# Kernel optimization log

Hardware: AMD Instinct MI355X
Metric: run time of the kernel (lower is better)

The kernel has to match this reference:

```python
import jax, jax.numpy as jnp
import numpy as np

ALPHA = 0.5  # default alpha of convex_ssd_chunk_forward
B_SZ, H, CS, DH, DS = 16, 32, 256, 64, 128


def setup_inputs() -> dict:
    key = jax.random.key(0)
    k1, k2, k3, k4, k5 = jax.random.split(key, 5)
    # A_chunk holds per-step log-decays; must be <= 0 so exp(cumsum) stays bounded.
    A_chunk = -jax.random.uniform(k2, (B_SZ, H, CS), dtype=jnp.float32) * 0.1
    return {
        "X_chunk": jax.random.normal(k1, (B_SZ, H, CS, DH), dtype=jnp.float32),
        "A_chunk": A_chunk,
        "B_chunk": jax.random.normal(k3, (B_SZ, H, CS, DS), dtype=jnp.float32),
        "C_chunk": jax.random.normal(k4, (B_SZ, H, CS, DS), dtype=jnp.float32),
        "h_prev": jax.random.normal(k5, (B_SZ, H, DS, DH), dtype=jnp.float32),
    }


def reference(X_chunk, A_chunk, B_chunk, C_chunk, h_prev):
    # Mamba2 SSD chunk scan with convex-combination state update.
    # X_chunk: [b,h,cs,dh], A_chunk: [b,h,cs], B/C_chunk: [b,h,cs,ds], h_prev: [b,h,ds,dh]
    cs = X_chunk.shape[2]
    A_cumsum = jnp.cumsum(A_chunk, axis=-1)                      # [b,h,cs]
    # Causal decay matrix L[i,j] = exp(Acum[i]-Acum[j]) for i>=j, else 0.
    diff = A_cumsum[..., :, None] - A_cumsum[..., None, :]       # [b,h,cs,cs]
    causal = jnp.tril(jnp.ones((cs, cs), dtype=bool))
    L = jnp.where(causal, jnp.exp(diff), 0.0)
    CB = jnp.einsum('bhid,bhjd->bhij', C_chunk, B_chunk)         # [b,h,cs,cs]
    Y_intra = jnp.einsum('bhij,bhjd->bhid', L * CB, X_chunk)     # [b,h,cs,dh]
    decay_to_end = jnp.exp(A_cumsum[:, :, -1:] - A_cumsum)       # [b,h,cs]
    h_chunk_contrib = jnp.einsum('bhts,bhtd,bht->bhsd', B_chunk, X_chunk, decay_to_end)  # [b,h,ds,dh]
    decay_total = jnp.exp(A_cumsum[:, :, -1])                    # [b,h]
    h_prev_decayed = decay_total[..., None, None] * h_prev
    h_end = ALPHA * h_prev_decayed + (1.0 - ALPHA) * h_chunk_contrib
    decay_from_start = jnp.exp(A_cumsum)                         # [b,h,cs]
    Y_inter = ALPHA * jnp.einsum('bhis,bhsd,bhi->bhid', C_chunk, h_prev, decay_from_start)
    Y_chunk = (1.0 - ALPHA) * Y_intra + Y_inter                  # [b,h,cs,dh]
    return Y_chunk, h_end, decay_total
```

## Files before the change

### kernel.cpp

```cpp
#include <hip/hip_runtime.h>

typedef __attribute__((ext_vector_type(8))) short s16x8;
typedef __attribute__((ext_vector_type(4))) float f32x4;
typedef __attribute__((ext_vector_type(4))) unsigned u32x4;

namespace {
constexpr int kCS = 256, kDH = 64, kDS = 128, kBH = 512;
constexpr float kAlpha = 0.5f;

constexpr int OFF_AC   = 0;
constexpr int OFF_ENEG = 1024;
constexpr int OFF_B    = 2048;
constexpr int OFF_BLO  = OFF_B + 8192;
constexpr int OFF_XT   = OFF_B + 16384;
constexpr int OFF_XTLO = OFF_XT + 4096;
constexpr int OFF_S    = OFF_XTLO + 4096;
constexpr int LDS_BYTES = OFF_S + 8192;

constexpr int HOFF_BT   = 2048;
constexpr int HOFF_BTLO = HOFF_BT + 8192;
constexpr int HOFF_XT   = HOFF_BT + 16384;
constexpr int HOFF_XTLO = HOFF_XT + 4096;
}

union F4 { float4 v; float f[4]; };

__device__ __forceinline__ unsigned cvt_pk_bf16(float a, float b) {
  unsigned r;
  asm("v_cvt_pk_bf16_f32 %0, %1, %2" : "=v"(r) : "v"(a), "v"(b));
  return r;
}

__device__ __forceinline__ unsigned short bf16_1(float x) {
  return (unsigned short)cvt_pk_bf16(x, x);
}

__device__ __forceinline__ void split2(float a, float b, unsigned& h, unsigned& l) {
  h = cvt_pk_bf16(a, b);
  l = cvt_pk_bf16(a - __uint_as_float(h << 16), b - __uint_as_float(h & 0xFFFF0000u));
}

__device__ __forceinline__ void split8v(float4 a, float4 b, s16x8& hi, s16x8& lo) {
  unsigned h0, h1, h2, h3, l0, l1, l2, l3;
  split2(a.x, a.y, h0, l0);
  split2(a.z, a.w, h1, l1);
  split2(b.x, b.y, h2, l2);
  split2(b.z, b.w, h3, l3);
  u32x4 H = {h0, h1, h2, h3}, L = {l0, l1, l2, l3};
  hi = __builtin_bit_cast(s16x8, H);
  lo = __builtin_bit_cast(s16x8, L);
}

__device__ __forceinline__ void split8s(float x0, float x1, float x2, float x3,
                                        float x4, float x5, float x6, float x7,
                                        s16x8& hi, s16x8& lo) {
  unsigned h0, h1, h2, h3, l0, l1, l2, l3;
  split2(x0, x1, h0, l0);
  split2(x2, x3, h1, l1);
  split2(x4, x5, h2, l2);
  split2(x6, x7, h3, l3);
  u32x4 H = {h0, h1, h2, h3}, L = {l0, l1, l2, l3};
  hi = __builtin_bit_cast(s16x8, H);
  lo = __builtin_bit_cast(s16x8, L);
}

__device__ __forceinline__ void lds_barrier() {
  asm volatile("s_waitcnt lgkmcnt(0)" ::: "memory");
  __builtin_amdgcn_s_barrier();
  __builtin_amdgcn_sched_barrier(0);
}

__global__ __launch_bounds__(512, 4) void fused_kernel(
    const float* __restrict__ Xg, const float* __restrict__ Ag,
    const float* __restrict__ Bg, const float* __restrict__ Cg,
    const float* __restrict__ Hg, float* __restrict__ Yg,
    float* __restrict__ hend, float* __restrict__ dtot) {
  __shared__ __align__(16) char smem[LDS_BYTES];
  const int bidx = blockIdx.x;
  const int tid = threadIdx.x;
  const int lane = tid & 63;
  const int w = tid >> 6;
  const int fr = lane & 15;
  const int fg = lane >> 4;

  const int swz = (bidx & 7) * 192 + (bidx >> 3);
  const int role = swz % 3;
  const int bh = swz / 3;

  const float* Xb = Xg + (size_t)bh * kCS * kDH;
  const float* Ab = Ag + (size_t)bh * kCS;
  const float* Bb = Bg + (size_t)bh * kCS * kDS;
  const float* Hb = Hg + (size_t)bh * kDS * kDH;

  if (role == 2) {
    float* ac   = (float*)(smem + OFF_AC);
    short* BThi = (short*)(smem + HOFF_BT);
    short* BTlo = (short*)(smem + HOFF_BTLO);
    short* XThi = (short*)(smem + HOFF_XT);
    short* XTlo = (short*)(smem + HOFF_XTLO);
    float* Ob = hend + (size_t)bh * kDS * kDH;

    float v = 0.f;
    if (tid < 256) {
      v = Ab[tid];
#pragma unroll
      for (int off = 1; off < 64; off <<= 1) {
        float t = __shfl_up(v, off);
        if (lane >= off) v += t;
      }
      float* wsum = (float*)(smem + HOFF_BT);
      if (lane == 63) wsum[w] = v;
    }
    __syncthreads();
    if (tid < 256) {
      const float* wsum = (const float*)(smem + HOFF_BT);
      float base = 0.f;
#pragma unroll
      for (int k = 0; k < 4; ++k)
        if (k < w) base += wsum[k];
      ac[tid] = v + base;
    }
    __syncthreads();
    const float alast = ac[kCS - 1];
    if (tid == 0) dtot[bh] = __expf(alast);

    f32x4 acc[4];
#pragma unroll
    for (int dg = 0; dg < 4; ++dg)
#pragma unroll
      for (int r = 0; r < 4; ++r) acc[dg][r] = 0.f;

    const int sblk = tid & 31;
    const int tq = (tid >> 5) & 7;
    const int st = w * 16 + fr;

    for (int t0 = 0; t0 < kCS; t0 += 32) {
      if (tid < 256) {
        F4 hr[4];
#pragma unroll
        for (int r = 0; r < 4; ++r)
          hr[r].v = *(const float4*)&Bb[(size_t)(t0 + tq * 4 + r) * kDS + sblk * 4];
#pragma unroll
        for (int c = 0; c < 4; ++c) {
          const int s2 = sblk * 4 + c;
          unsigned h0, h1, l0, l1;
          split2(hr[0].f[c], hr[1].f[c], h0, l0);
          split2(hr[2].f[c], hr[3].f[c], h1, l1);
          const int off = s2 * 32 + (((tq >> 1) ^ ((s2 >> 2) & 3)) << 3) + ((tq & 1) << 2);
          ((unsigned*)&BThi[off])[0] = h0;
          ((unsigned*)&BThi[off])[1] = h1;
          ((unsigned*)&BTlo[off])[0] = l0;
          ((unsigned*)&BTlo[off])[1] = l1;
        }
      } else {
        const int t2 = tid - 256;
        const int d = t2 & 63;
        const int wx = t2 >> 6;
        const float* xp = &Xb[(size_t)(t0 + wx * 8) * kDH + d];
        const float* ap = &ac[t0 + wx * 8];
        float w0 = __expf(alast - ap[0]), w1 = __expf(alast - ap[1]);
        float w2 = __expf(alast - ap[2]), w3 = __expf(alast - ap[3]);
        float w4 = __expf(alast - ap[4]), w5 = __expf(alast - ap[5]);
        float w6 = __expf(alast - ap[6]), w7 = __expf(alast - ap[7]);
        s16x8 h8, l8;
        split8s(xp[0 * kDH] * w0, xp[1 * kDH] * w1, xp[2 * kDH] * w2, xp[3 * kDH] * w3,
                xp[4 * kDH] * w4, xp[5 * kDH] * w5, xp[6 * kDH] * w6, xp[7 * kDH] * w7,
                h8, l8);
        const int off = d * 32 + ((wx ^ ((d >> 2) & 3)) << 3);
        *(s16x8*)&XThi[off] = h8;
        *(s16x8*)&XTlo[off] = l8;
      }
      __syncthreads();
      const int aoff = st * 32 + ((fg ^ ((st >> 2) & 3)) << 3);
      s16x8 ah = *(const s16x8*)&BThi[aoff];
      s16x8 al = *(const s16x8*)&BTlo[aoff];
#pragma unroll
      for (int dg = 0; dg < 4; ++dg) {
        const int drow = dg * 16 + fr;
        const int xoff = drow * 32 + ((fg ^ ((drow >> 2) & 3)) << 3);
        s16x8 xh = *(const s16x8*)&XThi[xoff];
        s16x8 xl = *(const s16x8*)&XTlo[xoff];
        acc[dg] = __builtin_amdgcn_mfma_f32_16x16x32_bf16(ah, xh, acc[dg], 0, 0, 0);
        acc[dg] = __builtin_amdgcn_mfma_f32_16x16x32_bf16(ah, xl, acc[dg], 0, 0, 0);
        acc[dg] = __builtin_amdgcn_mfma_f32_16x16x32_bf16(al, xh, acc[dg], 0, 0, 0);
      }
      __syncthreads();
    }
    const float dscale = kAlpha * __expf(alast);
    const float sc = 1.f - kAlpha;
#pragma unroll
    for (int dg = 0; dg < 4; ++dg) {
#pragma unroll
      for (int r = 0; r < 4; ++r) {
        const int s = w * 16 + fg * 4 + r;
        const int d = dg * 16 + fr;
        Ob[(size_t)s * kDH + d] = dscale * Hb[(size_t)s * kDH + d] + sc * acc[dg][r];
      }
    }
    return;
  }

  const int itA = role;
  const int itB = 3 - role;
  const int i0A = itA * 64, i0B = itB * 64;
  const int jt_n = 2 * itB + 2;
  const int jtA_n = 2 * itA + 2;
  const bool gB = w >= 4;
  const int wl = w & 3;
  const int i0g = gB ? i0B : i0A;

  float* ac   = (float*)(smem + OFF_AC);
  float* eneg = (float*)(smem + OFF_ENEG);
  short* Bhi  = (short*)(smem + OFF_B);
  short* Blo  = (short*)(smem + OFF_BLO);
  short* XThi = (short*)(smem + OFF_XT);
  short* XTlo = (short*)(smem + OFF_XTLO);
  short* Sall = (short*)(smem + OFF_S);
  float* CbA  = (float*)(smem + OFF_B);
  float* CbB  = (float*)(smem + OFF_XT);
  short* HThi = (short*)(smem + OFF_B);
  short* HTlo = (short*)(smem + OFF_XT);

  const float* Cg_b = Cg + (size_t)bh * kCS * kDS;
  float* Yb = Yg + (size_t)bh * kCS * kDH;

  {
    float v = 0.f;
    if (tid < 256) {
      v = Ab[tid];
#pragma unroll
      for (int off = 1; off < 64; off <<= 1) {
        float t = __shfl_up(v, off);
        if (lane >= off) v += t;
      }
      float* wsum = (float*)(smem + OFF_S);
      if (lane == 63) wsum[w] = v;
    }
    __syncthreads();
    if (tid < 256) {
      const float* wsum = (const float*)(smem + OFF_S);
      float base = 0.f;
#pragma unroll
      for (int k = 0; k < 4; ++k)
        if (k < w) base += wsum[k];
      const float a = v + base;
      ac[tid] = a;
      eneg[tid] = __expf(-a);
    }
    __syncthreads();
  }

  float eaci[4];
#pragma unroll
  for (int r = 0; r < 4; ++r) eaci[r] = __expf(ac[i0g + wl * 16 + fg * 4 + r]);

  const int prow = (tid >> 4) & 15;
  const int pg = tid & 15;
  const int xd = (tid - 256) & 63;
  const int xw = ((tid - 256) >> 6) & 3;
  float4 pb0, pb1, pb2, pb3;
  float px0, px1, px2, px3, px4, px5, px6, px7;
  if (tid < 256) {
    pb0 = *(const float4*)&Bb[(size_t)prow * kDS + pg * 8];
    pb1 = *(const float4*)&Bb[(size_t)prow * kDS + pg * 8 + 4];
    pb2 = *(const float4*)&Bb[(size_t)(16 + prow) * kDS + pg * 8];
    pb3 = *(const float4*)&Bb[(size_t)(16 + prow) * kDS + pg * 8 + 4];
  } else {
    const float* xp = &Xb[(size_t)(xw * 8) * kDH + xd];
    px0 = xp[0 * kDH]; px1 = xp[1 * kDH]; px2 = xp[2 * kDH]; px3 = xp[3 * kDH];
    px4 = xp[4 * kDH]; px5 = xp[5 * kDH]; px6 = xp[6 * kDH]; px7 = xp[7 * kDH];
  }

  s16x8 chi[4], clo[4];
#pragma unroll
  for (int m = 0; m < 2; ++m) {
#pragma unroll
    for (int k = 0; k < 2; ++k) {
      int fid = k * 512 + tid;
      int r = fid >> 5, c = fid & 31;
      *(float4*)&CbA[r * 128 + ((c ^ (r & 7)) << 2)] =
          *(const float4*)&Cg_b[(size_t)(i0A + m * 32 + r) * kDS + c * 4];
      *(float4*)&CbB[r * 128 + ((c ^ (r & 7)) << 2)] =
          *(const float4*)&Cg_b[(size_t)(i0B + m * 32 + r) * kDS + c * 4];
    }
    __syncthreads();
    if ((wl >> 1) == m) {
      const int lrow = (wl & 1) * 16 + fr;
      const float* crow = (gB ? CbB : CbA) + lrow * 128;
      const int r7 = lrow & 7;
#pragma unroll
      for (int kc = 0; kc < 4; ++kc) {
        const int c0 = kc * 8 + fg * 2;
        F4 u0, u1;
        u0.v = *(const float4*)&crow[(c0 ^ r7) << 2];
        u1.v = *(const float4*)&crow[((c0 + 1) ^ r7) << 2];
        split8v(u0.v, u1.v, chi[kc], clo[kc]);
      }
    }
    __syncthreads();
  }

  f32x4 yacc[4];
#pragma unroll
  for (int n = 0; n < 4; ++n)
#pragma unroll
    for (int r = 0; r < 4; ++r) yacc[n][r] = 0.f;

  short* Sp = Sall + w * 512;

  for (int jt = 0; jt < jt_n; ++jt) {
    if (tid < 256) {
      s16x8 h8, l8;
      split8v(pb0, pb1, h8, l8);
      int col = (pg ^ (prow & 7)) * 8;
      *(s16x8*)&Bhi[prow * 128 + col] = h8;
      *(s16x8*)&Blo[prow * 128 + col] = l8;
      const int row1 = 16 + prow;
      split8v(pb2, pb3, h8, l8);
      col = (pg ^ (row1 & 7)) * 8;
      *(s16x8*)&Bhi[row1 * 128 + col] = h8;
      *(s16x8*)&Blo[row1 * 128 + col] = l8;
    } else {
      s16x8 h8, l8;
      split8s(px0, px1, px2, px3, px4, px5, px6, px7, h8, l8);
      const int off = xd * 32 + ((xw ^ ((xd >> 2) & 3)) << 3);
      *(s16x8*)&XThi[off] = h8;
      *(s16x8*)&XTlo[off] = l8;
    }
    if (jt + 1 < jt_n) {
      const int j0n = (jt + 1) * 32;
      if (tid < 256) {
        pb0 = *(const float4*)&Bb[(size_t)(j0n + prow) * kDS + pg * 8];
        pb1 = *(const float4*)&Bb[(size_t)(j0n + prow) * kDS + pg * 8 + 4];
        pb2 = *(const float4*)&Bb[(size_t)(j0n + 16 + prow) * kDS + pg * 8];
        pb3 = *(const float4*)&Bb[(size_t)(j0n + 16 + prow) * kDS + pg * 8 + 4];
      } else {
        const float* xp = &Xb[(size_t)(j0n + xw * 8) * kDH + xd];
        px0 = xp[0 * kDH]; px1 = xp[1 * kDH]; px2 = xp[2 * kDH]; px3 = xp[3 * kDH];
        px4 = xp[4 * kDH]; px5 = xp[5 * kDH]; px6 = xp[6 * kDH]; px7 = xp[7 * kDH];
      }
    }
    lds_barrier();

    if (gB || jt < jtA_n) {
      const int j0 = jt * 32;
      f32x4 sA[2], sB[2];
#pragma unroll
      for (int n = 0; n < 2; ++n) {
#pragma unroll
        for (int r = 0; r < 4; ++r) { sA[n][r] = 0.f; sB[n][r] = 0.f; }
        const int jrow = n * 16 + fr;
        const short* bph = &Bhi[jrow * 128];
        const short* bpl = &Blo[jrow * 128];
#pragma unroll
        for (int kc = 0; kc < 2; ++kc) {
          const int phys = ((4 * kc + fg) ^ (jrow & 7)) * 8;
          s16x8 b8 = *(const s16x8*)&bph[phys];
          s16x8 l8 = *(const s16x8*)&bpl[phys];
          sA[n] = __builtin_amdgcn_mfma_f32_16x16x32_bf16(chi[kc], b8, sA[n], 0, 0, 0);
          sA[n] = __builtin_amdgcn_mfma_f32_16x16x32_bf16(chi[kc], l8, sA[n], 0, 0, 0);
          sA[n] = __builtin_amdgcn_mfma_f32_16x16x32_bf16(clo[kc], b8, sA[n], 0, 0, 0);
        }
#pragma unroll
        for (int kc = 2; kc < 4; ++kc) {
          const int phys = ((4 * kc + fg) ^ (jrow & 7)) * 8;
          s16x8 b8 = *(const s16x8*)&bph[phys];
          s16x8 l8 = *(const s16x8*)&bpl[phys];
          sB[n] = __builtin_amdgcn_mfma_f32_16x16x32_bf16(chi[kc], b8, sB[n], 0, 0, 0);
          sB[n] = __builtin_amdgcn_mfma_f32_16x16x32_bf16(chi[kc], l8, sB[n], 0, 0, 0);
          sB[n] = __builtin_amdgcn_mfma_f32_16x16x32_bf16(clo[kc], b8, sB[n], 0, 0, 0);
        }
      }
#pragma unroll
      for (int n = 0; n < 2; ++n) {
        const int jg = j0 + n * 16 + fr;
        const float enj = eneg[jg];
#pragma unroll
        for (int r = 0; r < 4; ++r) {
          const int iwl = fg * 4 + r;
          const int ig = i0g + wl * 16 + iwl;
          float sv = (sA[n][r] + sB[n][r]) * eaci[r] * enj;
          sv = (jg <= ig) ? sv : 0.f;
          Sp[iwl * 32 + (((n * 2 + (fr >> 3)) ^ fg) << 3) + (fr & 7)] = (short)bf16_1(sv);
        }
      }
      {
        s16x8 sa = *(const s16x8*)&Sp[fr * 32 + ((fg ^ (fr >> 2)) << 3)];
#pragma unroll
        for (int n = 0; n < 4; ++n) {
          const int drow = n * 16 + fr;
          const int pxo = (fg ^ ((drow >> 2) & 3)) << 3;
          s16x8 xh = *(const s16x8*)&XThi[drow * 32 + pxo];
          s16x8 xl = *(const s16x8*)&XTlo[drow * 32 + pxo];
          yacc[n] = __builtin_amdgcn_mfma_f32_16x16x32_bf16(sa, xh, yacc[n], 0, 0, 0);
          yacc[n] = __builtin_amdgcn_mfma_f32_16x16x32_bf16(sa, xl, yacc[n], 0, 0, 0);
        }
      }
    }
    lds_barrier();
  }

  {
    const int dd = tid & 15, tt = tid >> 4;
    F4 hr[4];
#pragma unroll
    for (int r = 0; r < 4; ++r)
      hr[r].v = *(const float4*)&Hb[(size_t)(tt * 4 + r) * kDH + dd * 4];
#pragma unroll
    for (int c = 0; c < 4; ++c) {
      const int d = dd * 4 + c;
      unsigned h0, h1, l0, l1;
      split2(hr[0].f[c], hr[1].f[c], h0, l0);
      split2(hr[2].f[c], hr[3].f[c], h1, l1);
      const int off = d * 128 + (((tt >> 1) ^ (d & 7)) << 3) + ((tt & 1) << 2);
      ((unsigned*)&HThi[off])[0] = h0;
      ((unsigned*)&HThi[off])[1] = h1;
      ((unsigned*)&HTlo[off])[0] = l0;
      ((unsigned*)&HTlo[off])[1] = l1;
    }
  }
  __syncthreads();

  f32x4 yh[4];
#pragma unroll
  for (int n = 0; n < 4; ++n)
#pragma unroll
    for (int r = 0; r < 4; ++r) yh[n][r] = 0.f;

#pragma unroll
  for (int kc = 0; kc < 4; ++kc) {
#pragma unroll
    for (int n = 0; n < 4; ++n) {
      const int drow = n * 16 + fr;
      const int phys = ((4 * kc + fg) ^ (drow & 7)) * 8;
      s16x8 hh = *(const s16x8*)&HThi[drow * 128 + phys];
      s16x8 hl = *(const s16x8*)&HTlo[drow * 128 + phys];
      yh[n] = __builtin_amdgcn_mfma_f32_16x16x32_bf16(chi[kc], hh, yh[n], 0, 0, 0);
      yh[n] = __builtin_amdgcn_mfma_f32_16x16x32_bf16(chi[kc], hl, yh[n], 0, 0, 0);
      yh[n] = __builtin_amdgcn_mfma_f32_16x16x32_bf16(clo[kc], hh, yh[n], 0, 0, 0);
    }
  }

#pragma unroll
  for (int n = 0; n < 4; ++n) {
#pragma unroll
    for (int r = 0; r < 4; ++r) {
      const int ig = i0g + wl * 16 + fg * 4 + r;
      const int d = n * 16 + fr;
      Yb[(size_t)ig * kDH + d] = (1.f - kAlpha) * yacc[n][r] + (kAlpha * eaci[r]) * yh[n][r];
    }
  }
}

extern "C" void kernel_launch(void* const* d_in, const int* in_sizes, int n_in,
                              void* d_out, int out_size, void* d_ws, size_t ws_size,
                              hipStream_t stream) {
  const float* X = (const float*)d_in[0];
  const float* A = (const float*)d_in[1];
  const float* B = (const float*)d_in[2];
  const float* C = (const float*)d_in[3];
  const float* H = (const float*)d_in[4];
  float* out = (float*)d_out;
  float* Y = out;
  float* hend = Y + (size_t)kBH * kCS * kDH;
  float* dt = hend + (size_t)kBH * kDS * kDH;

  fused_kernel<<<1536, 512, 0, stream>>>(X, A, B, C, H, Y, hend, dt);
}
```

Before: 79.57 us.

## Merge Y row-tile blocks into one block per head with 32-row warp tiles

Replaces the three-role split, where two Y blocks each took two 64-row tiles per head plus one h_end block, with a single Y block per head. Each warp now owns two 16-row groups, and warps are paired (rb = w or 11-w) to balance the causal triangle. C fragments load directly from global memory into registers instead of being staged through LDS, and B/X tiles are streamed across all 8 j-tiles by every thread. This cuts the grid from 1536 to 1024 blocks and avoids reloading B/X twice per head, at the cost of more registers per warp and a longer serial loop per block.

```diff
diff --git a/kernel.cpp b/kernel.cpp
--- a/kernel.cpp
+++ b/kernel.cpp
@@ -83,16 +83,15 @@
   const int fr = lane & 15;
   const int fg = lane >> 4;
 
-  const int swz = (bidx & 7) * 192 + (bidx >> 3);
-  const int role = swz % 3;
-  const int bh = swz / 3;
+  const int p = bidx & 511;
+  const int bh = (p & 7) * 64 + (p >> 3);
 
   const float* Xb = Xg + (size_t)bh * kCS * kDH;
   const float* Ab = Ag + (size_t)bh * kCS;
   const float* Bb = Bg + (size_t)bh * kCS * kDS;
   const float* Hb = Hg + (size_t)bh * kDS * kDH;
 
-  if (role == 2) {
+  if (bidx >= 512) {
     float* ac   = (float*)(smem + OFF_AC);
     short* BThi = (short*)(smem + HOFF_BT);
     short* BTlo = (short*)(smem + HOFF_BTLO);
@@ -200,14 +199,8 @@
     return;
   }
 
-  const int itA = role;
-  const int itB = 3 - role;
-  const int i0A = itA * 64, i0B = itB * 64;
-  const int jt_n = 2 * itB + 2;
-  const int jtA_n = 2 * itA + 2;
-  const bool gB = w >= 4;
-  const int wl = w & 3;
-  const int i0g = gB ? i0B : i0A;
+  const int rb = (w < 4) ? w : (11 - w);
+  const int i0g = rb * 32;
 
   float* ac   = (float*)(smem + OFF_AC);
   float* eneg = (float*)(smem + OFF_ENEG);
@@ -216,8 +209,6 @@
   short* XThi = (short*)(smem + OFF_XT);
   short* XTlo = (short*)(smem + OFF_XTLO);
   short* Sall = (short*)(smem + OFF_S);
-  float* CbA  = (float*)(smem + OFF_B);
-  float* CbB  = (float*)(smem + OFF_XT);
   short* HThi = (short*)(smem + OFF_B);
   short* HTlo = (short*)(smem + OFF_XT);
 
@@ -250,156 +241,138 @@
     __syncthreads();
   }
 
-  float eaci[4];
-#pragma unroll
-  for (int r = 0; r < 4; ++r) eaci[r] = __expf(ac[i0g + wl * 16 + fg * 4 + r]);
-
-  const int prow = (tid >> 4) & 15;
-  const int pg = tid & 15;
-  const int xd = (tid - 256) & 63;
-  const int xw = ((tid - 256) >> 6) & 3;
-  float4 pb0, pb1, pb2, pb3;
-  float px0, px1, px2, px3, px4, px5, px6, px7;
-  if (tid < 256) {
-    pb0 = *(const float4*)&Bb[(size_t)prow * kDS + pg * 8];
-    pb1 = *(const float4*)&Bb[(size_t)prow * kDS + pg * 8 + 4];
-    pb2 = *(const float4*)&Bb[(size_t)(16 + prow) * kDS + pg * 8];
-    pb3 = *(const float4*)&Bb[(size_t)(16 + prow) * kDS + pg * 8 + 4];
-  } else {
-    const float* xp = &Xb[(size_t)(xw * 8) * kDH + xd];
+  float eaci[2][4];
+#pragma unroll
+  for (int g = 0; g < 2; ++g)
+#pragma unroll
+    for (int r = 0; r < 4; ++r)
+      eaci[g][r] = __expf(ac[i0g + g * 16 + fg * 4 + r]);
+
+  s16x8 chi[2][4], clo[2][4];
+#pragma unroll
+  for (int g = 0; g < 2; ++g) {
+    const float* crow = &Cg_b[(size_t)(i0g + g * 16 + fr) * kDS];
+#pragma unroll
+    for (int kc = 0; kc < 4; ++kc) {
+      F4 u0, u1;
+      u0.v = *(const float4*)&crow[kc * 32 + fg * 8];
+      u1.v = *(const float4*)&crow[kc * 32 + fg * 8 + 4];
+      split8v(u0.v, u1.v, chi[g][kc], clo[g][kc]);
+    }
+  }
+
+  const int brow = tid >> 4;
+  const int bg = tid & 15;
+  const int xd = lane;
+  const int xq = w;
+  float4 pb0, pb1;
+  float px0, px1, px2, px3;
+  {
+    pb0 = *(const float4*)&Bb[(size_t)brow * kDS + bg * 8];
+    pb1 = *(const float4*)&Bb[(size_t)brow * kDS + bg * 8 + 4];
+    const float* xp = &Xb[(size_t)(xq * 4) * kDH + xd];
     px0 = xp[0 * kDH]; px1 = xp[1 * kDH]; px2 = xp[2 * kDH]; px3 = xp[3 * kDH];
-    px4 = xp[4 * kDH]; px5 = xp[5 * kDH]; px6 = xp[6 * kDH]; px7 = xp[7 * kDH];
-  }
-
-  s16x8 chi[4], clo[4];
-#pragma unroll
-  for (int m = 0; m < 2; ++m) {
-#pragma unroll
-    for (int k = 0; k < 2; ++k) {
-      int fid = k * 512 + tid;
-      int r = fid >> 5, c = fid & 31;
-      *(float4*)&CbA[r * 128 + ((c ^ (r & 7)) << 2)] =
-          *(const float4*)&Cg_b[(size_t)(i0A + m * 32 + r) * kDS + c * 4];
-      *(float4*)&CbB[r * 128 + ((c ^ (r & 7)) << 2)] =
-          *(const float4*)&Cg_b[(size_t)(i0B + m * 32 + r) * kDS + c * 4];
-    }
-    __syncthreads();
-    if ((wl >> 1) == m) {
-      const int lrow = (wl & 1) * 16 + fr;
-      const float* crow = (gB ? CbB : CbA) + lrow * 128;
-      const int r7 = lrow & 7;
-#pragma unroll
-      for (int kc = 0; kc < 4; ++kc) {
-        const int c0 = kc * 8 + fg * 2;
-        F4 u0, u1;
-        u0.v = *(const float4*)&crow[(c0 ^ r7) << 2];
-        u1.v = *(const float4*)&crow[((c0 + 1) ^ r7) << 2];
-        split8v(u0.v, u1.v, chi[kc], clo[kc]);
-      }
-    }
-    __syncthreads();
-  }
-
-  f32x4 yacc[4];
-#pragma unroll
-  for (int n = 0; n < 4; ++n)
-#pragma unroll
-    for (int r = 0; r < 4; ++r) yacc[n][r] = 0.f;
+  }
+
+  f32x4 yacc[2][4];
+#pragma unroll
+  for (int g = 0; g < 2; ++g)
+#pragma unroll
+    for (int n = 0; n < 4; ++n)
+#pragma unroll
+      for (int r = 0; r < 4; ++r) yacc[g][n][r] = 0.f;
 
   short* Sp = Sall + w * 512;
 
-  for (int jt = 0; jt < jt_n; ++jt) {
-    if (tid < 256) {
+  for (int jt = 0; jt < 8; ++jt) {
+    {
       s16x8 h8, l8;
       split8v(pb0, pb1, h8, l8);
-      int col = (pg ^ (prow & 7)) * 8;
-      *(s16x8*)&Bhi[prow * 128 + col] = h8;
-      *(s16x8*)&Blo[prow * 128 + col] = l8;
-      const int row1 = 16 + prow;
-      split8v(pb2, pb3, h8, l8);
-      col = (pg ^ (row1 & 7)) * 8;
-      *(s16x8*)&Bhi[row1 * 128 + col] = h8;
-      *(s16x8*)&Blo[row1 * 128 + col] = l8;
-    } else {
-      s16x8 h8, l8;
-      split8s(px0, px1, px2, px3, px4, px5, px6, px7, h8, l8);
-      const int off = xd * 32 + ((xw ^ ((xd >> 2) & 3)) << 3);
-      *(s16x8*)&XThi[off] = h8;
-      *(s16x8*)&XTlo[off] = l8;
-    }
-    if (jt + 1 < jt_n) {
+      const int col = (bg ^ (brow & 7)) * 8;
+      *(s16x8*)&Bhi[brow * 128 + col] = h8;
+      *(s16x8*)&Blo[brow * 128 + col] = l8;
+    }
+    {
+      unsigned h0, h1, l0, l1;
+      split2(px0, px1, h0, l0);
+      split2(px2, px3, h1, l1);
+      const int off = xd * 32 + (((xq >> 1) ^ ((xd >> 2) & 3)) << 3) + ((xq & 1) << 2);
+      ((unsigned*)&XThi[off])[0] = h0;
+      ((unsigned*)&XThi[off])[1] = h1;
+      ((unsigned*)&XTlo[off])[0] = l0;
+      ((unsigned*)&XTlo[off])[1] = l1;
+    }
+    if (jt + 1 < 8) {
       const int j0n = (jt + 1) * 32;
-      if (tid < 256) {
-        pb0 = *(const float4*)&Bb[(size_t)(j0n + prow) * kDS + pg * 8];
-        pb1 = *(const float4*)&Bb[(size_t)(j0n + prow) * kDS + pg * 8 + 4];
-        pb2 = *(const float4*)&Bb[(size_t)(j0n + 16 + prow) * kDS + pg * 8];
-        pb3 = *(const float4*)&Bb[(size_t)(j0n + 16 + prow) * kDS + pg * 8 + 4];
-      } else {
-        const float* xp = &Xb[(size_t)(j0n + xw * 8) * kDH + xd];
-        px0 = xp[0 * kDH]; px1 = xp[1 * kDH]; px2 = xp[2 * kDH]; px3 = xp[3 * kDH];
-        px4 = xp[4 * kDH]; px5 = xp[5 * kDH]; px6 = xp[6 * kDH]; px7 = xp[7 * kDH];
-      }
+      pb0 = *(const float4*)&Bb[(size_t)(j0n + brow) * kDS + bg * 8];
+      pb1 = *(const float4*)&Bb[(size_t)(j0n + brow) * kDS + bg * 8 + 4];
+      const float* xp = &Xb[(size_t)(j0n + xq * 4) * kDH + xd];
+      px0 = xp[0 * kDH]; px1 = xp[1 * kDH]; px2 = xp[2 * kDH]; px3 = xp[3 * kDH];
     }
     lds_barrier();
 
-    if (gB || jt < jtA_n) {
+    if (rb >= jt) {
       const int j0 = jt * 32;
-      f32x4 sA[2], sB[2];
-#pragma unroll
-      for (int n = 0; n < 2; ++n) {
-#pragma unroll
-        for (int r = 0; r < 4; ++r) { sA[n][r] = 0.f; sB[n][r] = 0.f; }
-        const int jrow = n * 16 + fr;
-        const short* bph = &Bhi[jrow * 128];
-        const short* bpl = &Blo[jrow * 128];
-#pragma unroll
-        for (int kc = 0; kc < 2; ++kc) {
-          const int phys = ((4 * kc + fg) ^ (jrow & 7)) * 8;
-          s16x8 b8 = *(const s16x8*)&bph[phys];
-          s16x8 l8 = *(const s16x8*)&bpl[phys];
-          sA[n] = __builtin_amdgcn_mfma_f32_16x16x32_bf16(chi[kc], b8, sA[n], 0, 0, 0);
-          sA[n] = __builtin_amdgcn_mfma_f32_16x16x32_bf16(chi[kc], l8, sA[n], 0, 0, 0);
-          sA[n] = __builtin_amdgcn_mfma_f32_16x16x32_bf16(clo[kc], b8, sA[n], 0, 0, 0);
+#pragma unroll
+      for (int g = 0; g < 2; ++g) {
+        f32x4 sA[2], sB[2];
+#pragma unroll
+        for (int n = 0; n < 2; ++n) {
+#pragma unroll
+          for (int r = 0; r < 4; ++r) { sA[n][r] = 0.f; sB[n][r] = 0.f; }
+          const int jrow = n * 16 + fr;
+          const short* bph = &Bhi[jrow * 128];
+          const short* bpl = &Blo[jrow * 128];
+#pragma unroll
+          for (int kc = 0; kc < 2; ++kc) {
+            const int phys = ((4 * kc + fg) ^ (jrow & 7)) * 8;
+            s16x8 b8 = *(const s16x8*)&bph[phys];
+            s16x8 l8 = *(const s16x8*)&bpl[phys];
+            sA[n] = __builtin_amdgcn_mfma_f32_16x16x32_bf16(chi[g][kc], b8, sA[n], 0, 0, 0);
+            sA[n] = __builtin_amdgcn_mfma_f32_16x16x32_bf16(chi[g][kc], l8, sA[n], 0, 0, 0);
+            sA[n] = __builtin_amdgcn_mfma_f32_16x16x32_bf16(clo[g][kc], b8, sA[n], 0, 0, 0);
+          }
+#pragma unroll
+          for (int kc = 2; kc < 4; ++kc) {
+            const int phys = ((4 * kc + fg) ^ (jrow & 7)) * 8;
+            s16x8 b8 = *(const s16x8*)&bph[phys];
+            s16x8 l8 = *(const s16x8*)&bpl[phys];
+            sB[n] = __builtin_amdgcn_mfma_f32_16x16x32_bf16(chi[g][kc], b8, sB[n], 0, 0, 0);
+            sB[n] = __builtin_amdgcn_mfma_f32_16x16x32_bf16(chi[g][kc], l8, sB[n], 0, 0, 0);
+            sB[n] = __builtin_amdgcn_mfma_f32_16x16x32_bf16(clo[g][kc], b8, sB[n], 0, 0, 0);
+          }
         }
 #pragma unroll
-        for (int kc = 2; kc < 4; ++kc) {
-          const int phys = ((4 * kc + fg) ^ (jrow & 7)) * 8;
-          s16x8 b8 = *(const s16x8*)&bph[phys];
-          s16x8 l8 = *(const s16x8*)&bpl[phys];
-          sB[n] = __builtin_amdgcn_mfma_f32_16x16x32_bf16(chi[kc], b8, sB[n], 0, 0, 0);
-          sB[n] = __builtin_amdgcn_mfma_f32_16x16x32_bf16(chi[kc], l8, sB[n], 0, 0, 0);
-          sB[n] = __builtin_amdgcn_mfma_f32_16x16x32_bf16(clo[kc], b8, sB[n], 0, 0, 0);
+        for (int n = 0; n < 2; ++n) {
+          const int jg = j0 + n * 16 + fr;
+          const float enj = eneg[jg];
+#pragma unroll
+          for (int r = 0; r < 4; ++r) {
+            const int iwl = fg * 4 + r;
+            const int ig = i0g + g * 16 + iwl;
+            float sv = (sA[n][r] + sB[n][r]) * eaci[g][r] * enj;
+            sv = (jg <= ig) ? sv : 0.f;
+            Sp[iwl * 32 + (((n * 2 + (fr >> 3)) ^ fg) << 3) + (fr & 7)] = (short)bf16_1(sv);
+          }
         }
-      }
-#pragma unroll
-      for (int n = 0; n < 2; ++n) {
-        const int jg = j0 + n * 16 + fr;
-        const float enj = eneg[jg];
-#pragma unroll
-        for (int r = 0; r < 4; ++r) {
-          const int iwl = fg * 4 + r;
-          const int ig = i0g + wl * 16 + iwl;
-          float sv = (sA[n][r] + sB[n][r]) * eaci[r] * enj;
-          sv = (jg <= ig) ? sv : 0.f;
-          Sp[iwl * 32 + (((n * 2 + (fr >> 3)) ^ fg) << 3) + (fr & 7)] = (short)bf16_1(sv);
+        {
+          s16x8 sa = *(const s16x8*)&Sp[fr * 32 + ((fg ^ (fr >> 2)) << 3)];
+#pragma unroll
+          for (int n = 0; n < 4; ++n) {
+            const int drow = n * 16 + fr;
+            const int pxo = (fg ^ ((drow >> 2) & 3)) << 3;
+            s16x8 xh = *(const s16x8*)&XThi[drow * 32 + pxo];
+            s16x8 xl = *(const s16x8*)&XTlo[drow * 32 + pxo];
+            yacc[g][n] = __builtin_amdgcn_mfma_f32_16x16x32_bf16(sa, xh, yacc[g][n], 0, 0, 0);
+            yacc[g][n] = __builtin_amdgcn_mfma_f32_16x16x32_bf16(sa, xl, yacc[g][n], 0, 0, 0);
+          }
         }
       }
-      {
-        s16x8 sa = *(const s16x8*)&Sp[fr * 32 + ((fg ^ (fr >> 2)) << 3)];
-#pragma unroll
-        for (int n = 0; n < 4; ++n) {
-          const int drow = n * 16 + fr;
-          const int pxo = (fg ^ ((drow >> 2) & 3)) << 3;
-          s16x8 xh = *(const s16x8*)&XThi[drow * 32 + pxo];
-          s16x8 xl = *(const s16x8*)&XTlo[drow * 32 + pxo];
-          yacc[n] = __builtin_amdgcn_mfma_f32_16x16x32_bf16(sa, xh, yacc[n], 0, 0, 0);
-          yacc[n] = __builtin_amdgcn_mfma_f32_16x16x32_bf16(sa, xl, yacc[n], 0, 0, 0);
-        }
-      }
     }
     lds_barrier();
   }
 
+  __syncthreads();
   {
     const int dd = tid & 15, tt = tid >> 4;
     F4 hr[4];
@@ -421,33 +394,34 @@
   }
   __syncthreads();
 
-  f32x4 yh[4];
-#pragma unroll
-  for (int n = 0; n < 4; ++n)
-#pragma unroll
-    for (int r = 0; r < 4; ++r) yh[n][r] = 0.f;
-
-#pragma unroll
-  for (int kc = 0; kc < 4; ++kc) {
+#pragma unroll
+  for (int g = 0; g < 2; ++g) {
+    f32x4 yh[4];
+#pragma unroll
+    for (int n = 0; n < 4; ++n)
+#pragma unroll
+      for (int r = 0; r < 4; ++r) yh[n][r] = 0.f;
+#pragma unroll
+    for (int kc = 0; kc < 4; ++kc) {
+#pragma unroll
+      for (int n = 0; n < 4; ++n) {
+        const int drow = n * 16 + fr;
+        const int phys = ((4 * kc + fg) ^ (drow & 7)) * 8;
+        s16x8 hh = *(const s16x8*)&HThi[drow * 128 + phys];
+        s16x8 hl = *(const s16x8*)&HTlo[drow * 128 + phys];
+        yh[n] = __builtin_amdgcn_mfma_f32_16x16x32_bf16(chi[g][kc], hh, yh[n], 0, 0, 0);
+        yh[n] = __builtin_amdgcn_mfma_f32_16x16x32_bf16(chi[g][kc], hl, yh[n], 0, 0, 0);
+        yh[n] = __builtin_amdgcn_mfma_f32_16x16x32_bf16(clo[g][kc], hh, yh[n], 0, 0, 0);
+      }
+    }
 #pragma unroll
     for (int n = 0; n < 4; ++n) {
-      const int drow = n * 16 + fr;
-      const int phys = ((4 * kc + fg) ^ (drow & 7)) * 8;
-      s16x8 hh = *(const s16x8*)&HThi[drow * 128 + phys];
-      s16x8 hl = *(const s16x8*)&HTlo[drow * 128 + phys];
-      yh[n] = __builtin_amdgcn_mfma_f32_16x16x32_bf16(chi[kc], hh, yh[n], 0, 0, 0);
-      yh[n] = __builtin_amdgcn_mfma_f32_16x16x32_bf16(chi[kc], hl, yh[n], 0, 0, 0);
-      yh[n] = __builtin_amdgcn_mfma_f32_16x16x32_bf16(clo[kc], hh, yh[n], 0, 0, 0);
-    }
-  }
-
-#pragma unroll
-  for (int n = 0; n < 4; ++n) {
-#pragma unroll
-    for (int r = 0; r < 4; ++r) {
-      const int ig = i0g + wl * 16 + fg * 4 + r;
-      const int d = n * 16 + fr;
-      Yb[(size_t)ig * kDH + d] = (1.f - kAlpha) * yacc[n][r] + (kAlpha * eaci[r]) * yh[n][r];
+#pragma unroll
+      for (int r = 0; r < 4; ++r) {
+        const int ig = i0g + g * 16 + fg * 4 + r;
+        const int d = n * 16 + fr;
+        Yb[(size_t)ig * kDH + d] = (1.f - kAlpha) * yacc[g][n][r] + (kAlpha * eaci[g][r]) * yh[n][r];
+      }
     }
   }
 }
@@ -465,5 +439,5 @@
   float* hend = Y + (size_t)kBH * kCS * kDH;
   float* dt = hend + (size_t)kBH * kDS * kDH;
 
-  fused_kernel<<<1536, 512, 0, stream>>>(X, A, B, C, H, Y, hend, dt);
-}
+  fused_kernel<<<1024, 512, 0, stream>>>(X, A, B, C, H, Y, hend, dt);
+}
```

Measured after the change: 152.1 us. 91.2% more time.
